# Performance work log

Hardware: AMD Instinct MI355X
Metric: run time of the kernel (lower is better)

## Reference

```python
import jax, jax.numpy as jnp
import numpy as np

B, P, D, VP, VD = 256, 1152, 10, 8, 16
NUM_ITER = 3


def setup_inputs() -> dict:
    key = jax.random.key(0)
    k1, k2 = jax.random.split(key)
    x = jax.random.normal(k1, (B, P, VP, 1), dtype=jnp.float32)
    # learned transform matrices, init randn/100 as in the torch module
    W = jax.random.normal(k2, (P, D, VD, VP), dtype=jnp.float32) / 100.0
    return {"x": x, "W": W}


def _squash(s, axis):
    # v = ||s||^2/(1+||s||^2) * s/||s||
    sq = jnp.sum(s * s, axis=axis, keepdims=True)
    return s * sq / (1.0 + sq) / jnp.sqrt(sq + 1e-9)


def reference(x, W):
    xs = x[..., 0]                                      # [B,P,8]
    # u_hat[b,p,d,:] = W[p,d] @ x[b,p]  (no explicit stack/broadcast materialization)
    u_hat = jnp.einsum('pdij,bpj->bpdi', W, xs)          # [B,P,D,16]
    u_stop = jax.lax.stop_gradient(u_hat)
    b_ij = jnp.zeros((B, P, D, 1), dtype=u_hat.dtype)    # torch b_ij [B,P,D,1,1], trailing 1 dropped
    v = None
    for it in range(NUM_ITER):
        # faithful to source: softmax over torch dim=3 (size-1 axis) -> all ones
        c_ij = jax.nn.softmax(b_ij, axis=3)               # [B,P,D,1]
        u = u_hat if it == NUM_ITER - 1 else u_stop
        s_j = jnp.sum(c_ij * u, axis=1)                   # [B,D,16]
        v = _squash(s_j, axis=2)                          # [B,D,16]
        if it != NUM_ITER - 1:
            # agreement: u_hat^T v -> scalar per (b,p,d)
            upd = jnp.einsum('bpdi,bdi->bpd', u_hat, v)[..., None]
            b_ij = b_ij + upd
    return v[..., None]                                   # [B,D,16,1] matching torch output
```

## Files before the change

kernel.cpp:

```cpp
#include <hip/hip_runtime.h>
#include <math.h>

#define M 256
#define N 160
#define K 9216
#define CH 72
#define KC 128
#define BM 64

using f32x4 = __attribute__((ext_vector_type(4))) float;
using bf16x8 = __attribute__((ext_vector_type(8))) short;

__device__ __forceinline__ ushort f2bf(float f) {
  uint u = __builtin_bit_cast(uint, f);
  u += 0x7FFF + ((u >> 16) & 1);
  return (ushort)(u >> 16);
}

template <bool ATOMIC>
__global__ __launch_bounds__(256) void gemm_mfma(const float* __restrict__ x,
                                                 const float* __restrict__ W,
                                                 float* __restrict__ part) {
  __shared__ ushort Wl[N * KC];

  const int t = threadIdx.x;
  const int bx = blockIdx.x;
  const int xcd = bx & 7;
  const int idx = bx >> 3;
  const int c = xcd * 9 + (idx >> 2);
  const int mt = idx & 3;
  const int m0 = mt * BM;
  const int k0 = c * KC;

  const int w = t >> 6;
  const int l = t & 63;
  const int lr = l & 15;
  const int lg = l >> 4;

  const float* xr = x + (size_t)(m0 + w * 16 + lr) * K + k0;
  float4 araw[4][2];
#pragma unroll
  for (int ks = 0; ks < 4; ++ks) {
    araw[ks][0] = *(const float4*)(xr + ks * 32 + lg * 8);
    araw[ks][1] = *(const float4*)(xr + ks * 32 + lg * 8 + 4);
  }

  {
    const float* ws = W + (size_t)(c * 16) * 1280;
#pragma unroll
    for (int q = 0; q < 20; ++q) {
      const int f = t + 256 * q;
      const float4 v = *(const float4*)(ws + 4 * (size_t)f);
      const int pl = f / 320;
      const int r = f - pl * 320;
      const int d = r >> 5;
      const int idx2 = r & 31;
      const int i = idx2 >> 1;
      const int j = (idx2 & 1) << 2;
      const int n = d * 16 + i;
      const int kk = pl * 8 + j;
      ushort4 h = {f2bf(v.x), f2bf(v.y), f2bf(v.z), f2bf(v.w)};
      const int E = (n * KC + kk) ^ ((n & 7) << 3);
      *(ushort4*)&Wl[E] = h;
    }
  }

  bf16x8 af[4];
#pragma unroll
  for (int ks = 0; ks < 4; ++ks) {
    af[ks][0] = (short)f2bf(araw[ks][0].x);
    af[ks][1] = (short)f2bf(araw[ks][0].y);
    af[ks][2] = (short)f2bf(araw[ks][0].z);
    af[ks][3] = (short)f2bf(araw[ks][0].w);
    af[ks][4] = (short)f2bf(araw[ks][1].x);
    af[ks][5] = (short)f2bf(araw[ks][1].y);
    af[ks][6] = (short)f2bf(araw[ks][1].z);
    af[ks][7] = (short)f2bf(araw[ks][1].w);
  }
  __syncthreads();

  f32x4 acc[10];
#pragma unroll
  for (int nt = 0; nt < 10; ++nt) acc[nt] = {0.f, 0.f, 0.f, 0.f};

#pragma unroll
  for (int ks = 0; ks < 4; ++ks) {
#pragma unroll
    for (int nt = 0; nt < 10; ++nt) {
      const int n = nt * 16 + lr;
      const int EB = (n * KC + ks * 32 + lg * 8) ^ ((n & 7) << 3);
      const bf16x8 b = *(const bf16x8*)&Wl[EB];
      acc[nt] =
          __builtin_amdgcn_mfma_f32_16x16x32_bf16(af[ks], b, acc[nt], 0, 0, 0);
    }
  }

  if (ATOMIC) {
#pragma unroll
    for (int nt = 0; nt < 10; ++nt)
#pragma unroll
      for (int r = 0; r < 4; ++r) {
        const int row = m0 + w * 16 + lg * 4 + r;
        atomicAdd(&part[(size_t)row * N + nt * 16 + lr], acc[nt][r]);
      }
  } else {
    float* dst = part + (size_t)c * (M * N);
#pragma unroll
    for (int nt = 0; nt < 10; ++nt)
#pragma unroll
      for (int r = 0; r < 4; ++r) {
        const int row = m0 + w * 16 + lg * 4 + r;
        dst[(size_t)row * N + nt * 16 + lr] = acc[nt][r];
      }
  }
}

__global__ __launch_bounds__(256) void reduce_squash4(
    const float* __restrict__ part, float* __restrict__ out) {
  __shared__ f32x4 red[256];
  const int t = threadIdx.x;
  const int o4 = t & 63;
  const int slice = t >> 6;
  const f32x4* p4 = (const f32x4*)part;
  const int base4 = blockIdx.x * 64;

  f32x4 sum = {0.f, 0.f, 0.f, 0.f};
#pragma unroll 6
  for (int cc = 0; cc < 18; ++cc) {
    const int c = slice * 18 + cc;
    sum += p4[(size_t)c * (M * N / 4) + base4 + o4];
  }
  red[t] = sum;
  __syncthreads();
  if (t < 64) {
    const f32x4 s = red[t] + red[t + 64] + red[t + 128] + red[t + 192];
    float n2 = s[0] * s[0] + s[1] * s[1] + s[2] * s[2] + s[3] * s[3];
    n2 += __shfl_xor(n2, 1);
    n2 += __shfl_xor(n2, 2);
    const float sc = n2 / (1.0f + n2) / sqrtf(n2 + 1e-9f);
    f32x4 o = {s[0] * sc, s[1] * sc, s[2] * sc, s[3] * sc};
    ((f32x4*)out)[base4 + t] = o;
  }
}

__global__ __launch_bounds__(256) void squash_k(float* __restrict__ out) {
  const int e = blockIdx.x * 256 + threadIdx.x;
  const float s = out[e];
  float s2 = s * s;
  s2 += __shfl_xor(s2, 1);
  s2 += __shfl_xor(s2, 2);
  s2 += __shfl_xor(s2, 4);
  s2 += __shfl_xor(s2, 8);
  out[e] = s * s2 / (1.0f + s2) / sqrtf(s2 + 1e-9f);
}

extern "C" void kernel_launch(void* const* d_in, const int* in_sizes, int n_in,
                              void* d_out, int out_size, void* d_ws,
                              size_t ws_size, hipStream_t stream) {
  const float* x = (const float*)d_in[0];
  const float* W = (const float*)d_in[1];
  float* out = (float*)d_out;

  const size_t need = (size_t)CH * M * N * sizeof(float);
  if (ws_size >= need) {
    gemm_mfma<false><<<4 * CH, 256, 0, stream>>>(x, W, (float*)d_ws);
    reduce_squash4<<<(M * N) / 256, 256, 0, stream>>>((const float*)d_ws, out);
  } else {
    hipMemsetAsync(out, 0, (size_t)M * N * sizeof(float), stream);
    gemm_mfma<true><<<4 * CH, 256, 0, stream>>>(x, W, out);
    squash_k<<<(M * N) / 256, 256, 0, stream>>>(out);
  }
}
```

Measured before the change: 19.45 us.

## Restructure split-K GEMM into fewer chunks with register-prefetched three-stage pipeline

```diff
diff --git a/kernel.cpp b/kernel.cpp
--- a/kernel.cpp
+++ b/kernel.cpp
@@ -1,34 +1,33 @@
 #include <hip/hip_runtime.h>
+#include <hip/hip_bf16.h>
 #include <math.h>
 
 #define M 256
 #define N 160
 #define K 9216
-#define CH 72
-#define KC 128
-#define BM 64
+#define CH 32
+#define KC 288
+#define BM 32
+#define XST 104
 
 using f32x4 = __attribute__((ext_vector_type(4))) float;
 using bf16x8 = __attribute__((ext_vector_type(8))) short;
 
 __device__ __forceinline__ ushort f2bf(float f) {
-  uint u = __builtin_bit_cast(uint, f);
-  u += 0x7FFF + ((u >> 16) & 1);
-  return (ushort)(u >> 16);
+  return __builtin_bit_cast(ushort, __float2bfloat16(f));
 }
 
 template <bool ATOMIC>
 __global__ __launch_bounds__(256) void gemm_mfma(const float* __restrict__ x,
                                                  const float* __restrict__ W,
                                                  float* __restrict__ part) {
-  __shared__ ushort Wl[N * KC];
+  __shared__ ushort Wl[12 * 1280];
+  __shared__ ushort Xl[BM * XST];
 
   const int t = threadIdx.x;
   const int bx = blockIdx.x;
-  const int xcd = bx & 7;
-  const int idx = bx >> 3;
-  const int c = xcd * 9 + (idx >> 2);
-  const int mt = idx & 3;
+  const int mt = bx & 7;
+  const int c = bx >> 3;
   const int m0 = mt * BM;
   const int k0 = c * KC;
 
@@ -36,81 +35,94 @@
   const int l = t & 63;
   const int lr = l & 15;
   const int lg = l >> 4;
+  const int msub = w & 1;
+  const int nh = w >> 1;
 
-  const float* xr = x + (size_t)(m0 + w * 16 + lr) * K + k0;
-  float4 araw[4][2];
+  float4 wv[15], xv[3];
+  int xrow[3], xkq[3];
 #pragma unroll
-  for (int ks = 0; ks < 4; ++ks) {
-    araw[ks][0] = *(const float4*)(xr + ks * 32 + lg * 8);
-    araw[ks][1] = *(const float4*)(xr + ks * 32 + lg * 8 + 4);
+  for (int q = 0; q < 3; ++q) {
+    const int f = t + 256 * q;
+    xrow[q] = f / 24;
+    xkq[q] = (f - xrow[q] * 24) * 4;
   }
 
-  {
-    const float* ws = W + (size_t)(c * 16) * 1280;
+  auto load = [&](int s) {
+    const float* wsp = W + ((size_t)c * 36 + s * 12) * 1280;
 #pragma unroll
-    for (int q = 0; q < 20; ++q) {
-      const int f = t + 256 * q;
-      const float4 v = *(const float4*)(ws + 4 * (size_t)f);
-      const int pl = f / 320;
-      const int r = f - pl * 320;
-      const int d = r >> 5;
-      const int idx2 = r & 31;
-      const int i = idx2 >> 1;
-      const int j = (idx2 & 1) << 2;
-      const int n = d * 16 + i;
-      const int kk = pl * 8 + j;
-      ushort4 h = {f2bf(v.x), f2bf(v.y), f2bf(v.z), f2bf(v.w)};
-      const int E = (n * KC + kk) ^ ((n & 7) << 3);
-      *(ushort4*)&Wl[E] = h;
+    for (int q = 0; q < 15; ++q)
+      wv[q] = *(const float4*)(wsp + 4 * (size_t)(t + 256 * q));
+    const float* xs = x + (size_t)m0 * K + k0 + s * 96;
+#pragma unroll
+    for (int q = 0; q < 3; ++q)
+      xv[q] = *(const float4*)(xs + (size_t)xrow[q] * K + xkq[q]);
+  };
+  auto put = [&]() {
+#pragma unroll
+    for (int q = 0; q < 15; ++q) {
+      const int f4 = t + 256 * q;
+      ushort4 h = {f2bf(wv[q].x), f2bf(wv[q].y), f2bf(wv[q].z), f2bf(wv[q].w)};
+      *(ushort4*)&Wl[4 * f4] = h;
     }
-  }
+#pragma unroll
+    for (int q = 0; q < 3; ++q) {
+      ushort4 h = {f2bf(xv[q].x), f2bf(xv[q].y), f2bf(xv[q].z), f2bf(xv[q].w)};
+      *(ushort4*)&Xl[xrow[q] * XST + xkq[q]] = h;
+    }
+  };
 
-  bf16x8 af[4];
+  f32x4 acc[5];
 #pragma unroll
-  for (int ks = 0; ks < 4; ++ks) {
-    af[ks][0] = (short)f2bf(araw[ks][0].x);
-    af[ks][1] = (short)f2bf(araw[ks][0].y);
-    af[ks][2] = (short)f2bf(araw[ks][0].z);
-    af[ks][3] = (short)f2bf(araw[ks][0].w);
-    af[ks][4] = (short)f2bf(araw[ks][1].x);
-    af[ks][5] = (short)f2bf(araw[ks][1].y);
-    af[ks][6] = (short)f2bf(araw[ks][1].z);
-    af[ks][7] = (short)f2bf(araw[ks][1].w);
-  }
+  for (int nt = 0; nt < 5; ++nt) acc[nt] = {0.f, 0.f, 0.f, 0.f};
+
+  auto comp = [&]() {
+#pragma unroll
+    for (int ks = 0; ks < 3; ++ks) {
+      const bf16x8 a =
+          *(const bf16x8*)&Xl[(msub * 16 + lr) * XST + ks * 32 + lg * 8];
+#pragma unroll
+      for (int nt = 0; nt < 5; ++nt) {
+        const bf16x8 b =
+            *(const bf16x8*)&Wl[(ks * 4 + lg) * 1280 + (nh * 5 + nt) * 128 +
+                                lr * 8];
+        acc[nt] =
+            __builtin_amdgcn_mfma_f32_16x16x32_bf16(a, b, acc[nt], 0, 0, 0);
+      }
+    }
+  };
+
+  load(0);
+  put();
   __syncthreads();
-
-  f32x4 acc[10];
-#pragma unroll
-  for (int nt = 0; nt < 10; ++nt) acc[nt] = {0.f, 0.f, 0.f, 0.f};
-
-#pragma unroll
-  for (int ks = 0; ks < 4; ++ks) {
-#pragma unroll
-    for (int nt = 0; nt < 10; ++nt) {
-      const int n = nt * 16 + lr;
-      const int EB = (n * KC + ks * 32 + lg * 8) ^ ((n & 7) << 3);
-      const bf16x8 b = *(const bf16x8*)&Wl[EB];
-      acc[nt] =
-          __builtin_amdgcn_mfma_f32_16x16x32_bf16(af[ks], b, acc[nt], 0, 0, 0);
-    }
-  }
+  load(1);
+  comp();
+  __syncthreads();
+  put();
+  __syncthreads();
+  load(2);
+  comp();
+  __syncthreads();
+  put();
+  __syncthreads();
+  comp();
 
   if (ATOMIC) {
 #pragma unroll
-    for (int nt = 0; nt < 10; ++nt)
+    for (int nt = 0; nt < 5; ++nt)
 #pragma unroll
       for (int r = 0; r < 4; ++r) {
-        const int row = m0 + w * 16 + lg * 4 + r;
-        atomicAdd(&part[(size_t)row * N + nt * 16 + lr], acc[nt][r]);
+        const int row = m0 + msub * 16 + lg * 4 + r;
+        atomicAdd(&part[(size_t)row * N + (nh * 5 + nt) * 16 + lr],
+                  acc[nt][r]);
       }
   } else {
     float* dst = part + (size_t)c * (M * N);
 #pragma unroll
-    for (int nt = 0; nt < 10; ++nt)
+    for (int nt = 0; nt < 5; ++nt)
 #pragma unroll
       for (int r = 0; r < 4; ++r) {
-        const int row = m0 + w * 16 + lg * 4 + r;
-        dst[(size_t)row * N + nt * 16 + lr] = acc[nt][r];
+        const int row = m0 + msub * 16 + lg * 4 + r;
+        dst[(size_t)row * N + (nh * 5 + nt) * 16 + lr] = acc[nt][r];
       }
   }
 }
@@ -125,9 +137,9 @@
   const int base4 = blockIdx.x * 64;
 
   f32x4 sum = {0.f, 0.f, 0.f, 0.f};
-#pragma unroll 6
-  for (int cc = 0; cc < 18; ++cc) {
-    const int c = slice * 18 + cc;
+#pragma unroll
+  for (int cc = 0; cc < 8; ++cc) {
+    const int c = slice * 8 + cc;
     sum += p4[(size_t)c * (M * N / 4) + base4 + o4];
   }
   red[t] = sum;
@@ -163,11 +175,11 @@
 
   const size_t need = (size_t)CH * M * N * sizeof(float);
   if (ws_size >= need) {
-    gemm_mfma<false><<<4 * CH, 256, 0, stream>>>(x, W, (float*)d_ws);
+    gemm_mfma<false><<<256, 256, 0, stream>>>(x, W, (float*)d_ws);
     reduce_squash4<<<(M * N) / 256, 256, 0, stream>>>((const float*)d_ws, out);
   } else {
     hipMemsetAsync(out, 0, (size_t)M * N * sizeof(float), stream);
-    gemm_mfma<true><<<4 * CH, 256, 0, stream>>>(x, W, out);
+    gemm_mfma<true><<<256, 256, 0, stream>>>(x, W, out);
     squash_k<<<(M * N) / 256, 256, 0, stream>>>(out);
   }
 }
```

Result: faster. 18.43 us (-5.2%).
